# Kernel optimization log

Measured on AMD Instinct MI355X. Metric: run time of the kernel, lower is better.

The kernel has to match this reference:

```python
import jax, jax.numpy as jnp
import numpy as np

T, D_IN, D_OUT, E = 8192, 1024, 1024, 8
LN_EPS = 1e-5


def setup_inputs() -> dict:
    key = jax.random.key(0)
    k1, k2, k3 = jax.random.split(key, 3)
    x = jax.random.normal(k1, (T, D_IN), dtype=jnp.float32)
    # tokens are pre-sorted by expert; equal load => capacity = T // E per expert
    expert_frequency = jnp.full((E,), T // E, dtype=jnp.int64)
    # per-expert Linear(input_dim, output_dim) params
    W = jax.random.normal(k2, (E, D_IN, D_OUT), dtype=jnp.float32) / np.sqrt(D_IN)
    b = jax.random.normal(k3, (E, D_OUT), dtype=jnp.float32) * 0.02
    # per-expert LayerNorm(output_dim) affine params
    ln_gamma = jnp.ones((E, D_OUT), dtype=jnp.float32)
    ln_beta = jnp.zeros((E, D_OUT), dtype=jnp.float32)
    return {
        "expert_ordered_input": x,
        "expert_frequency": expert_frequency,
        "W": W,
        "b": b,
        "ln_gamma": ln_gamma,
        "ln_beta": ln_beta,
    }


def reference(expert_ordered_input, expert_frequency, W, b, ln_gamma, ln_beta):
    # Grouped-GEMM form of: split tokens by expert_frequency, apply per-expert
    # LayerBlock (Linear -> relu -> LayerNorm), then concat along token dim.
    # Frequencies are equal (capacity = T // E), so the ragged split is a reshape.
    x = expert_ordered_input
    n_tok, d_in = x.shape
    n_exp = W.shape[0]
    cap = n_tok // n_exp  # static capacity per expert
    xe = x.reshape(n_exp, cap, d_in)                       # [E, cap, d_in]
    h = jnp.einsum("ecd,edf->ecf", xe, W) + b[:, None, :]  # [E, cap, d_out]
    h = jax.nn.relu(h)
    mu = jnp.mean(h, axis=-1, keepdims=True)
    var = jnp.var(h, axis=-1, keepdims=True)
    hn = (h - mu) * jax.lax.rsqrt(var + LN_EPS)
    out = hn * ln_gamma[:, None, :] + ln_beta[:, None, :]
    return out.reshape(n_tok, -1)                          # concat over experts
```

## Files before the change

### kernel.cpp

```cpp
#include <hip/hip_runtime.h>
#include <hip/hip_bf16.h>
#include <stdint.h>

#define T_TOK 8192
#define DIN   1024
#define DOUT  1024
#define NEXP  8
#define CAP   1024
#define LN_EPS 1e-5f

#define BM 128
#define BN 128
#define BK 32
#define LDSS 48

typedef __attribute__((ext_vector_type(8))) short short8;
typedef __attribute__((ext_vector_type(4))) float f32x4;

__device__ __forceinline__ unsigned short f2bf(float f) {
    union { float f; unsigned int u; } v; v.f = f;
    unsigned int u = v.u;
    unsigned int r = u + 0x7FFFu + ((u >> 16) & 1u);
    return (unsigned short)(r >> 16);
}

__global__ __launch_bounds__(256) void wt_kernel(const float* __restrict__ W,
                                                 unsigned short* __restrict__ Wt) {
    __shared__ float tile[32][33];
    int e  = blockIdx.z;
    int k0 = blockIdx.y * 32;
    int n0 = blockIdx.x * 32;
    const float* Wp = W + (size_t)e * DIN * DOUT;
    unsigned short* Wtp = Wt + (size_t)e * DIN * DOUT;
    int tx = threadIdx.x;
    int ty = threadIdx.y;
#pragma unroll
    for (int r = 0; r < 4; r++)
        tile[ty + r * 8][tx] = Wp[(size_t)(k0 + ty + r * 8) * DOUT + (n0 + tx)];
    __syncthreads();
#pragma unroll
    for (int r = 0; r < 4; r++)
        Wtp[(size_t)(n0 + ty + r * 8) * DIN + (k0 + tx)] = f2bf(tile[tx][ty + r * 8]);
}

__global__ __launch_bounds__(256, 2) void gemm_kernel(
    const float* __restrict__ X,
    const unsigned short* __restrict__ Wt,
    const float* __restrict__ Bias,
    float* __restrict__ H)
{
    __shared__ unsigned short As[BM * LDSS];
    __shared__ unsigned short Bs[BN * LDSS];

    int blk = blockIdx.x;
    int e   = blk >> 6;
    int tt  = blk & 63;
    int m0  = (tt >> 3) * BM;
    int n0  = (tt & 7) * BN;

    int tid  = threadIdx.x;
    int wave = tid >> 6;
    int lane = tid & 63;
    int wm   = (wave >> 1) * 64;
    int wn   = (wave & 1) * 64;
    int lrow = lane & 15;
    int quad = lane >> 4;

    const float* Xe = X + (size_t)(e * CAP + m0) * DIN;
    const unsigned short* We = Wt + (size_t)e * DOUT * DIN + (size_t)n0 * DIN;

    f32x4 acc[4][4];
#pragma unroll
    for (int i = 0; i < 4; i++)
#pragma unroll
        for (int j = 0; j < 4; j++)
            acc[i][j] = (f32x4)(0.0f);

    for (int k0 = 0; k0 < DIN; k0 += BK) {
#pragma unroll
        for (int i = 0; i < 4; i++) {
            int idx = tid + i * 256;
            int row = idx >> 3;
            int c4  = idx & 7;
            const float4 xv = *(const float4*)(Xe + (size_t)row * DIN + k0 + c4 * 4);
            ushort4 bv;
            bv.x = f2bf(xv.x); bv.y = f2bf(xv.y); bv.z = f2bf(xv.z); bv.w = f2bf(xv.w);
            *(ushort4*)&As[row * LDSS + c4 * 4] = bv;
        }
#pragma unroll
        for (int i = 0; i < 2; i++) {
            int idx = tid + i * 256;
            int row = idx >> 2;
            int c   = idx & 3;
            uint4 wv = *(const uint4*)(We + (size_t)row * DIN + k0 + c * 8);
            *(uint4*)&Bs[row * LDSS + c * 8] = wv;
        }
        __syncthreads();

        short8 af[4], bf[4];
#pragma unroll
        for (int i = 0; i < 4; i++)
            af[i] = *(const short8*)&As[(wm + i * 16 + lrow) * LDSS + quad * 8];
#pragma unroll
        for (int j = 0; j < 4; j++)
            bf[j] = *(const short8*)&Bs[(wn + j * 16 + lrow) * LDSS + quad * 8];
#pragma unroll
        for (int i = 0; i < 4; i++)
#pragma unroll
            for (int j = 0; j < 4; j++)
                acc[i][j] = __builtin_amdgcn_mfma_f32_16x16x32_bf16(af[i], bf[j], acc[i][j], 0, 0, 0);
        __syncthreads();
    }

    float bias[4];
#pragma unroll
    for (int j = 0; j < 4; j++)
        bias[j] = Bias[e * DOUT + n0 + wn + j * 16 + lrow];

    int tok0 = e * CAP + m0 + wm;
#pragma unroll
    for (int i = 0; i < 4; i++) {
#pragma unroll
        for (int j = 0; j < 4; j++) {
            int col = n0 + wn + j * 16 + lrow;
#pragma unroll
            for (int r = 0; r < 4; r++) {
                int row = tok0 + i * 16 + quad * 4 + r;
                float v = acc[i][j][r] + bias[j];
                v = fmaxf(v, 0.0f);
                H[(size_t)row * DOUT + col] = v;
            }
        }
    }
}

__global__ __launch_bounds__(256) void ln_kernel(float* __restrict__ H,
                                                 const float* __restrict__ G,
                                                 const float* __restrict__ Bt) {
    int row = blockIdx.x;
    int e   = row >> 10;
    int tid  = threadIdx.x;
    int wave = tid >> 6;
    int lane = tid & 63;
    float* hp = H + (size_t)row * DOUT;

    float4 x = *(const float4*)(hp + tid * 4);
    float s  = x.x + x.y + x.z + x.w;
    float ss = fmaf(x.x, x.x, fmaf(x.y, x.y, fmaf(x.z, x.z, x.w * x.w)));

#pragma unroll
    for (int m = 32; m >= 1; m >>= 1) {
        s  += __shfl_xor(s, m);
        ss += __shfl_xor(ss, m);
    }
    __shared__ float red[8];
    if (lane == 0) { red[wave] = s; red[4 + wave] = ss; }
    __syncthreads();
    float ts  = red[0] + red[1] + red[2] + red[3];
    float tss = red[4] + red[5] + red[6] + red[7];

    float mean = ts * (1.0f / DOUT);
    float var  = tss * (1.0f / DOUT) - mean * mean;
    var = fmaxf(var, 0.0f);
    float rs = rsqrtf(var + LN_EPS);

    float4 g = *(const float4*)(G  + (size_t)e * DOUT + tid * 4);
    float4 b = *(const float4*)(Bt + (size_t)e * DOUT + tid * 4);
    float4 y;
    y.x = (x.x - mean) * rs * g.x + b.x;
    y.y = (x.y - mean) * rs * g.y + b.y;
    y.z = (x.z - mean) * rs * g.z + b.z;
    y.w = (x.w - mean) * rs * g.w + b.w;
    *(float4*)(hp + tid * 4) = y;
}

extern "C" void kernel_launch(void* const* d_in, const int* in_sizes, int n_in,
                              void* d_out, int out_size, void* d_ws, size_t ws_size,
                              hipStream_t stream) {
    const float* x  = (const float*)d_in[0];
    const float* W  = (const float*)d_in[2];
    const float* b  = (const float*)d_in[3];
    const float* g  = (const float*)d_in[4];
    const float* be = (const float*)d_in[5];
    unsigned short* Wt = (unsigned short*)d_ws;
    float* out = (float*)d_out;

    dim3 tb(32, 8);
    dim3 tg(32, 32, 8);
    wt_kernel<<<tg, tb, 0, stream>>>(W, Wt);
    gemm_kernel<<<dim3(512), dim3(256), 0, stream>>>(x, Wt, b, out);
    ln_kernel<<<dim3(8192), dim3(256), 0, stream>>>(out, g, be);
}
```

Before: 163.4 us.

## Fuse GEMM with LayerNorm using full-row tiles and resident A in LDS

Replaces the separate GEMM and LayerNorm kernels with one kernel. Each 512-thread block owns 32 tokens across all 1024 output columns, keeps the bf16 A tile in swizzled LDS, streams B fragments directly from global memory, and reduces the row statistics in-block. This removes the round trip of H through global memory and one kernel launch. It also rewrites the weight transpose kernel to use float4 loads and ushort4 stores. In exchange only 256 blocks launch, B fragments are read uncached through L2 without LDS staging, and LDS usage per block is large, which may cut occupancy and MFMA feed rate.

```diff
diff --git a/kernel.cpp b/kernel.cpp
--- a/kernel.cpp
+++ b/kernel.cpp
@@ -9,11 +9,6 @@
 #define CAP   1024
 #define LN_EPS 1e-5f
 
-#define BM 128
-#define BN 128
-#define BK 32
-#define LDSS 48
-
 typedef __attribute__((ext_vector_type(8))) short short8;
 typedef __attribute__((ext_vector_type(4))) float f32x4;
 
@@ -27,151 +22,163 @@
 __global__ __launch_bounds__(256) void wt_kernel(const float* __restrict__ W,
                                                  unsigned short* __restrict__ Wt) {
     __shared__ float tile[32][33];
-    int e  = blockIdx.z;
-    int k0 = blockIdx.y * 32;
-    int n0 = blockIdx.x * 32;
+    int t  = blockIdx.x;
+    int e  = t >> 10;
+    int k0 = ((t >> 5) & 31) * 32;
+    int n0 = (t & 31) * 32;
+    int tid = threadIdx.x;
     const float* Wp = W + (size_t)e * DIN * DOUT;
     unsigned short* Wtp = Wt + (size_t)e * DIN * DOUT;
-    int tx = threadIdx.x;
-    int ty = threadIdx.y;
-#pragma unroll
-    for (int r = 0; r < 4; r++)
-        tile[ty + r * 8][tx] = Wp[(size_t)(k0 + ty + r * 8) * DOUT + (n0 + tx)];
-    __syncthreads();
-#pragma unroll
-    for (int r = 0; r < 4; r++)
-        Wtp[(size_t)(n0 + ty + r * 8) * DIN + (k0 + tx)] = f2bf(tile[tx][ty + r * 8]);
-}
-
-__global__ __launch_bounds__(256, 2) void gemm_kernel(
+    {
+        int k  = tid >> 3;
+        int c4 = tid & 7;
+        float4 v = *(const float4*)(Wp + (size_t)(k0 + k) * DOUT + n0 + c4 * 4);
+        tile[k][c4 * 4 + 0] = v.x; tile[k][c4 * 4 + 1] = v.y;
+        tile[k][c4 * 4 + 2] = v.z; tile[k][c4 * 4 + 3] = v.w;
+    }
+    __syncthreads();
+    {
+        int n  = tid >> 3;
+        int kc = tid & 7;
+        ushort4 o;
+        o.x = f2bf(tile[kc * 4 + 0][n]);
+        o.y = f2bf(tile[kc * 4 + 1][n]);
+        o.z = f2bf(tile[kc * 4 + 2][n]);
+        o.w = f2bf(tile[kc * 4 + 3][n]);
+        *(ushort4*)(Wtp + (size_t)(n0 + n) * DIN + k0 + kc * 4) = o;
+    }
+}
+
+__global__ __launch_bounds__(512, 2) void gemmln_kernel(
     const float* __restrict__ X,
     const unsigned short* __restrict__ Wt,
     const float* __restrict__ Bias,
-    float* __restrict__ H)
+    const float* __restrict__ G,
+    const float* __restrict__ Bt,
+    float* __restrict__ Out)
 {
-    __shared__ unsigned short As[BM * LDSS];
-    __shared__ unsigned short Bs[BN * LDSS];
+    __shared__ unsigned short As[32 * 1024];
 
     int blk = blockIdx.x;
-    int e   = blk >> 6;
-    int tt  = blk & 63;
-    int m0  = (tt >> 3) * BM;
-    int n0  = (tt & 7) * BN;
-
-    int tid  = threadIdx.x;
+    int tid = threadIdx.x;
+    int e   = blk & 7;
+    int m0  = (blk >> 3) * 32;
+
     int wave = tid >> 6;
     int lane = tid & 63;
-    int wm   = (wave >> 1) * 64;
-    int wn   = (wave & 1) * 64;
     int lrow = lane & 15;
     int quad = lane >> 4;
+    int wn   = wave * 128;
 
     const float* Xe = X + (size_t)(e * CAP + m0) * DIN;
-    const unsigned short* We = Wt + (size_t)e * DOUT * DIN + (size_t)n0 * DIN;
-
-    f32x4 acc[4][4];
-#pragma unroll
-    for (int i = 0; i < 4; i++)
-#pragma unroll
-        for (int j = 0; j < 4; j++)
+    const unsigned short* We = Wt + (size_t)e * DOUT * DIN;
+
+#pragma unroll
+    for (int it = 0; it < 16; it++) {
+        int f  = it * 512 + tid;
+        int r  = f >> 8;
+        int c4 = f & 255;
+        float4 v = ((const float4*)Xe)[f];
+        ushort4 o;
+        o.x = f2bf(v.x); o.y = f2bf(v.y); o.z = f2bf(v.z); o.w = f2bf(v.w);
+        int O    = c4 >> 1;
+        int half = c4 & 1;
+        int O2   = O ^ (r & 7);
+        *(ushort4*)&As[r * 1024 + O2 * 8 + half * 4] = o;
+    }
+    __syncthreads();
+
+    f32x4 acc[2][8];
+#pragma unroll
+    for (int i = 0; i < 2; i++)
+#pragma unroll
+        for (int j = 0; j < 8; j++)
             acc[i][j] = (f32x4)(0.0f);
 
-    for (int k0 = 0; k0 < DIN; k0 += BK) {
-#pragma unroll
-        for (int i = 0; i < 4; i++) {
-            int idx = tid + i * 256;
-            int row = idx >> 3;
-            int c4  = idx & 7;
-            const float4 xv = *(const float4*)(Xe + (size_t)row * DIN + k0 + c4 * 4);
-            ushort4 bv;
-            bv.x = f2bf(xv.x); bv.y = f2bf(xv.y); bv.z = f2bf(xv.z); bv.w = f2bf(xv.w);
-            *(ushort4*)&As[row * LDSS + c4 * 4] = bv;
-        }
+#pragma unroll 2
+    for (int k0 = 0; k0 < DIN; k0 += 32) {
+        short8 bf[8];
+#pragma unroll
+        for (int j = 0; j < 8; j++) {
+            int n = wn + j * 16 + lrow;
+            bf[j] = *(const short8*)(We + (size_t)n * DIN + k0 + quad * 8);
+        }
+        short8 af[2];
 #pragma unroll
         for (int i = 0; i < 2; i++) {
-            int idx = tid + i * 256;
-            int row = idx >> 2;
-            int c   = idx & 3;
-            uint4 wv = *(const uint4*)(We + (size_t)row * DIN + k0 + c * 8);
-            *(uint4*)&Bs[row * LDSS + c * 8] = wv;
-        }
-        __syncthreads();
-
-        short8 af[4], bf[4];
-#pragma unroll
-        for (int i = 0; i < 4; i++)
-            af[i] = *(const short8*)&As[(wm + i * 16 + lrow) * LDSS + quad * 8];
-#pragma unroll
-        for (int j = 0; j < 4; j++)
-            bf[j] = *(const short8*)&Bs[(wn + j * 16 + lrow) * LDSS + quad * 8];
-#pragma unroll
-        for (int i = 0; i < 4; i++)
-#pragma unroll
-            for (int j = 0; j < 4; j++)
-                acc[i][j] = __builtin_amdgcn_mfma_f32_16x16x32_bf16(af[i], bf[j], acc[i][j], 0, 0, 0);
-        __syncthreads();
-    }
-
-    float bias[4];
-#pragma unroll
-    for (int j = 0; j < 4; j++)
-        bias[j] = Bias[e * DOUT + n0 + wn + j * 16 + lrow];
-
-    int tok0 = e * CAP + m0 + wm;
-#pragma unroll
-    for (int i = 0; i < 4; i++) {
-#pragma unroll
-        for (int j = 0; j < 4; j++) {
-            int col = n0 + wn + j * 16 + lrow;
-#pragma unroll
-            for (int r = 0; r < 4; r++) {
-                int row = tok0 + i * 16 + quad * 4 + r;
-                float v = acc[i][j][r] + bias[j];
-                v = fmaxf(v, 0.0f);
-                H[(size_t)row * DOUT + col] = v;
+            int r  = i * 16 + lrow;
+            int O2 = ((k0 >> 3) + quad) ^ (r & 7);
+            af[i] = *(const short8*)&As[r * 1024 + O2 * 8];
+        }
+#pragma unroll
+        for (int j = 0; j < 8; j++) {
+            acc[0][j] = __builtin_amdgcn_mfma_f32_16x16x32_bf16(af[0], bf[j], acc[0][j], 0, 0, 0);
+            acc[1][j] = __builtin_amdgcn_mfma_f32_16x16x32_bf16(af[1], bf[j], acc[1][j], 0, 0, 0);
+        }
+    }
+
+    float bias[8], gg[8], bb[8];
+#pragma unroll
+    for (int j = 0; j < 8; j++) {
+        int col = e * DOUT + wn + j * 16 + lrow;
+        bias[j] = Bias[col];
+        gg[j]   = G[col];
+        bb[j]   = Bt[col];
+    }
+
+    __syncthreads();
+    float2* lnp = (float2*)As;
+    float2* mrs = ((float2*)As) + 256;
+
+#pragma unroll
+    for (int i = 0; i < 2; i++) {
+#pragma unroll
+        for (int r = 0; r < 4; r++) {
+            float s = 0.f, ss = 0.f;
+#pragma unroll
+            for (int j = 0; j < 8; j++) {
+                float v = fmaxf(acc[i][j][r] + bias[j], 0.f);
+                acc[i][j][r] = v;
+                s += v;
+                ss = fmaf(v, v, ss);
             }
-        }
-    }
-}
-
-__global__ __launch_bounds__(256) void ln_kernel(float* __restrict__ H,
-                                                 const float* __restrict__ G,
-                                                 const float* __restrict__ Bt) {
-    int row = blockIdx.x;
-    int e   = row >> 10;
-    int tid  = threadIdx.x;
-    int wave = tid >> 6;
-    int lane = tid & 63;
-    float* hp = H + (size_t)row * DOUT;
-
-    float4 x = *(const float4*)(hp + tid * 4);
-    float s  = x.x + x.y + x.z + x.w;
-    float ss = fmaf(x.x, x.x, fmaf(x.y, x.y, fmaf(x.z, x.z, x.w * x.w)));
-
-#pragma unroll
-    for (int m = 32; m >= 1; m >>= 1) {
-        s  += __shfl_xor(s, m);
-        ss += __shfl_xor(ss, m);
-    }
-    __shared__ float red[8];
-    if (lane == 0) { red[wave] = s; red[4 + wave] = ss; }
-    __syncthreads();
-    float ts  = red[0] + red[1] + red[2] + red[3];
-    float tss = red[4] + red[5] + red[6] + red[7];
-
-    float mean = ts * (1.0f / DOUT);
-    float var  = tss * (1.0f / DOUT) - mean * mean;
-    var = fmaxf(var, 0.0f);
-    float rs = rsqrtf(var + LN_EPS);
-
-    float4 g = *(const float4*)(G  + (size_t)e * DOUT + tid * 4);
-    float4 b = *(const float4*)(Bt + (size_t)e * DOUT + tid * 4);
-    float4 y;
-    y.x = (x.x - mean) * rs * g.x + b.x;
-    y.y = (x.y - mean) * rs * g.y + b.y;
-    y.z = (x.z - mean) * rs * g.z + b.z;
-    y.w = (x.w - mean) * rs * g.w + b.w;
-    *(float4*)(hp + tid * 4) = y;
+#pragma unroll
+            for (int m = 1; m <= 8; m <<= 1) {
+                s  += __shfl_xor(s, m);
+                ss += __shfl_xor(ss, m);
+            }
+            if (lrow == 0)
+                lnp[(i * 16 + quad * 4 + r) * 8 + wave] = make_float2(s, ss);
+        }
+    }
+    __syncthreads();
+    if (tid < 32) {
+        float s = 0.f, ss = 0.f;
+#pragma unroll
+        for (int w = 0; w < 8; w++) {
+            float2 p = lnp[tid * 8 + w];
+            s += p.x; ss += p.y;
+        }
+        float mu  = s * (1.0f / DOUT);
+        float var = fmaxf(ss * (1.0f / DOUT) - mu * mu, 0.f);
+        mrs[tid] = make_float2(mu, rsqrtf(var + LN_EPS));
+    }
+    __syncthreads();
+
+#pragma unroll
+    for (int i = 0; i < 2; i++) {
+#pragma unroll
+        for (int r = 0; r < 4; r++) {
+            int lr = i * 16 + quad * 4 + r;
+            float2 m = mrs[lr];
+            size_t grow = (size_t)(e * CAP + m0 + lr);
+#pragma unroll
+            for (int j = 0; j < 8; j++) {
+                int gcol = wn + j * 16 + lrow;
+                Out[grow * DOUT + gcol] = (acc[i][j][r] - m.x) * m.y * gg[j] + bb[j];
+            }
+        }
+    }
 }
 
 extern "C" void kernel_launch(void* const* d_in, const int* in_sizes, int n_in,
@@ -182,12 +189,13 @@
     const float* b  = (const float*)d_in[3];
     const float* g  = (const float*)d_in[4];
     const float* be = (const float*)d_in[5];
+    float* out = (float*)d_out;
+
+    const size_t WT_BYTES = (size_t)NEXP * DIN * DOUT * 2;
+    if (ws_size < WT_BYTES) return;
+
     unsigned short* Wt = (unsigned short*)d_ws;
-    float* out = (float*)d_out;
-
-    dim3 tb(32, 8);
-    dim3 tg(32, 32, 8);
-    wt_kernel<<<tg, tb, 0, stream>>>(W, Wt);
-    gemm_kernel<<<dim3(512), dim3(256), 0, stream>>>(x, Wt, b, out);
-    ln_kernel<<<dim3(8192), dim3(256), 0, stream>>>(out, g, be);
-}
+
+    wt_kernel<<<dim3(8192), dim3(256), 0, stream>>>(W, Wt);
+    gemmln_kernel<<<dim3(256), dim3(512), 0, stream>>>(x, Wt, b, g, be, out);
+}
```

New measurement: 171.7 us. 5.1% more time.
